# Optimization experiments

Hardware: AMD Instinct MI355X
Metric: run time of the kernel (lower is better)

## Reference

```python
import jax, jax.numpy as jnp
import numpy as np

SPATIAL_SHAPES = np.array([[128, 128], [64, 64], [32, 32], [16, 16]], dtype=np.int32)  # (H, W) per level
D_MODEL = 256
D_FFN = 1024
N_LEVELS = 4
N_HEADS = 8
N_POINTS = 4
HEAD_DIM = D_MODEL // N_HEADS
B = 2
LEN = int((SPATIAL_SHAPES[:, 0] * SPATIAL_SHAPES[:, 1]).sum())  # 21760


def layer_norm(x, g, b, eps=1e-5):
    mu = x.mean(-1, keepdims=True)
    var = ((x - mu) ** 2).mean(-1, keepdims=True)
    return (x - mu) / jnp.sqrt(var + eps) * g + b


def ms_deform_attn_core(value, sampling_locations, attention_weights):
    # value: [B, Len, M, D]; locations: [B, Lq, M, L, P, 2] in [0,1]; weights: [B, Lq, M, L, P]
    B_, _, M, D = value.shape
    Lq = sampling_locations.shape[1]
    P = sampling_locations.shape[4]
    out = jnp.zeros((B_, M, Lq, D), value.dtype)
    start = 0
    for lvl, (H, W) in enumerate(SPATIAL_SHAPES.tolist()):
        v = value[:, start:start + H * W].transpose(0, 2, 1, 3)  # [B, M, H*W, D]
        start += H * W
        loc = sampling_locations[:, :, :, lvl].transpose(0, 2, 1, 3, 4)  # [B, M, Lq, P, 2]
        # grid_sample semantics: align_corners=False, padding_mode='zeros'
        x = loc[..., 0] * W - 0.5
        y = loc[..., 1] * H - 0.5
        x0 = jnp.floor(x)
        y0 = jnp.floor(y)
        wx = (x - x0)[..., None]
        wy = (y - y0)[..., None]

        def gather(xi, yi):
            valid = ((xi >= 0) & (xi < W) & (yi >= 0) & (yi < H)).astype(value.dtype)
            idx = (jnp.clip(yi, 0, H - 1) * W + jnp.clip(xi, 0, W - 1)).astype(jnp.int32)
            idx = idx.reshape(B_, M, Lq * P)
            g = jnp.take_along_axis(v, idx[..., None], axis=2).reshape(B_, M, Lq, P, D)
            return g * valid[..., None]

        v00 = gather(x0, y0)
        v01 = gather(x0 + 1, y0)
        v10 = gather(x0, y0 + 1)
        v11 = gather(x0 + 1, y0 + 1)
        samp = (v00 * (1 - wx) + v01 * wx) * (1 - wy) + (v10 * (1 - wx) + v11 * wx) * wy
        w_l = attention_weights[:, :, :, lvl].transpose(0, 2, 1, 3)  # [B, M, Lq, P]
        out = out + (samp * w_l[..., None]).sum(axis=3)
    return out.transpose(0, 2, 1, 3).reshape(B_, Lq, M * D)


def setup_inputs() -> dict:
    key = jax.random.key(0)
    ks = jax.random.split(key, 16)
    f32 = jnp.float32

    def lin(k, fan_in, fan_out, scale=None):
        s = scale if scale is not None else 1.0 / np.sqrt(fan_in)
        return jax.random.normal(k, (fan_in, fan_out), f32) * s

    starts = np.concatenate([[0], np.cumsum(SPATIAL_SHAPES[:, 0] * SPATIAL_SHAPES[:, 1])[:-1]]).astype(np.int32)
    inp = {
        "src": jax.random.normal(ks[0], (B, LEN, D_MODEL), f32),
        "pos": jax.random.normal(ks[1], (B, LEN, D_MODEL), f32),
        "reference_points": jax.random.uniform(ks[2], (B, LEN, N_LEVELS, 2), f32),
        "spatial_shapes": jnp.asarray(SPATIAL_SHAPES),
        "level_start_index": jnp.asarray(starts),
        "norm1_g": jnp.ones((D_MODEL,), f32), "norm1_b": jnp.zeros((D_MODEL,), f32),
        "norm2_g": jnp.ones((D_MODEL,), f32), "norm2_b": jnp.zeros((D_MODEL,), f32),
        "W_value": lin(ks[3], D_MODEL, D_MODEL), "b_value": jnp.zeros((D_MODEL,), f32),
        "W_off": lin(ks[4], D_MODEL, N_HEADS * N_LEVELS * N_POINTS * 2, scale=0.01),
        "b_off": jax.random.normal(ks[5], (N_HEADS * N_LEVELS * N_POINTS * 2,), f32) * 0.01,
        "W_attn": lin(ks[6], D_MODEL, N_HEADS * N_LEVELS * N_POINTS),
        "b_attn": jnp.zeros((N_HEADS * N_LEVELS * N_POINTS,), f32),
        "W_out": lin(ks[7], D_MODEL, D_MODEL), "b_out": jnp.zeros((D_MODEL,), f32),
        "W_ffn1": lin(ks[8], D_MODEL, D_FFN), "b_ffn1": jnp.zeros((D_FFN,), f32),
        "W_ffn2": lin(ks[9], D_FFN, D_MODEL), "b_ffn2": jnp.zeros((D_MODEL,), f32),
    }
    return inp


def reference(src, pos, reference_points, spatial_shapes, level_start_index,
              norm1_g, norm1_b, norm2_g, norm2_b,
              W_value, b_value, W_off, b_off, W_attn, b_attn, W_out, b_out,
              W_ffn1, b_ffn1, W_ffn2, b_ffn2):
    B_, Lq, C = src.shape
    # pre-norm deformable self-attention; NOTE: value path uses un-normed src (faithful to source)
    q = layer_norm(src, norm1_g, norm1_b) + pos
    value = (src @ W_value + b_value).reshape(B_, Lq, N_HEADS, HEAD_DIM)
    offsets = (q @ W_off + b_off).reshape(B_, Lq, N_HEADS, N_LEVELS, N_POINTS, 2)
    attn = jax.nn.softmax((q @ W_attn + b_attn).reshape(B_, Lq, N_HEADS, N_LEVELS * N_POINTS), axis=-1)
    attn = attn.reshape(B_, Lq, N_HEADS, N_LEVELS, N_POINTS)
    offset_normalizer = spatial_shapes[..., ::-1].astype(src.dtype)  # (W, H) per level
    loc = reference_points[:, :, None, :, None, :] + offsets / offset_normalizer[None, None, None, :, None, :]
    attn_out = ms_deform_attn_core(value, loc, attn) @ W_out + b_out
    src = src + attn_out
    h = layer_norm(src, norm2_g, norm2_b)
    h = jax.nn.gelu(h @ W_ffn1 + b_ffn1, approximate=False) @ W_ffn2 + b_ffn2
    return src + h
```

## Files before the change

### kernel.cpp

```cpp
#include <hip/hip_runtime.h>
#include <hip/hip_bf16.h>
#include <math.h>

#define LEN_TOT 21760
#define BATCH 2
#define MROWS (BATCH * LEN_TOT)
#define DMODEL 256
#define DFFN 1024

typedef unsigned short ushort_t;
typedef __attribute__((ext_vector_type(8))) short short8;
typedef __attribute__((ext_vector_type(4))) float floatx4;
typedef __attribute__((address_space(3))) ushort_t lds_us;
typedef __attribute__((address_space(1))) const ushort_t glb_us;

__device__ __forceinline__ ushort_t f2b(float f) {
    unsigned u = __float_as_uint(f);
    unsigned r = (u + 0x7FFFu + ((u >> 16) & 1u)) >> 16;
    return (ushort_t)r;
}
__device__ __forceinline__ float b2f(ushort_t u) {
    return __uint_as_float(((unsigned)u) << 16);
}

struct TP {
    const float* s[6];
    ushort_t*    d[6];
    int K[6];
    int N[6];
    int start[7];
};

__global__ __launch_bounds__(256) void transpose_convert(TP tp) {
    __shared__ float tile[32][33];
    int blk = blockIdx.x;
    int seg = 0;
    while (seg < 5 && blk >= tp.start[seg + 1]) seg++;
    int local = blk - tp.start[seg];
    int K = tp.K[seg], N = tp.N[seg];
    int tn = N >> 5;
    int k0 = (local / tn) << 5, n0 = (local % tn) << 5;
    int r = threadIdx.x >> 5, c = threadIdx.x & 31;
    const float* src = tp.s[seg];
    #pragma unroll
    for (int rr = r; rr < 32; rr += 8)
        tile[rr][c] = src[(size_t)(k0 + rr) * N + n0 + c];
    __syncthreads();
    ushort_t* dst = tp.d[seg];
    #pragma unroll
    for (int rr = r; rr < 32; rr += 8)
        dst[(size_t)(n0 + rr) * K + k0 + c] = f2b(tile[c][rr]);
}

__global__ __launch_bounds__(256) void ln_dual_kernel(
    const float* __restrict__ x, const float* __restrict__ g,
    const float* __restrict__ bb, const float* __restrict__ addv,
    ushort_t* __restrict__ y_bf, ushort_t* __restrict__ x_bf)
{
    int row  = blockIdx.x * 4 + (threadIdx.x >> 6);
    int lane = threadIdx.x & 63;
    size_t base = (size_t)row * DMODEL + lane * 4;
    float4 v = *(const float4*)(x + base);

    float s = v.x + v.y + v.z + v.w;
    #pragma unroll
    for (int o = 32; o; o >>= 1) s += __shfl_xor(s, o, 64);
    float mu = s * (1.0f / 256.0f);

    float d0 = v.x - mu, d1 = v.y - mu, d2 = v.z - mu, d3 = v.w - mu;
    float vs = d0*d0 + d1*d1 + d2*d2 + d3*d3;
    #pragma unroll
    for (int o = 32; o; o >>= 1) vs += __shfl_xor(vs, o, 64);
    float rstd = rsqrtf(vs * (1.0f / 256.0f) + 1e-5f);

    float4 gv = *(const float4*)(g  + lane * 4);
    float4 bv = *(const float4*)(bb + lane * 4);
    float o0 = d0 * rstd * gv.x + bv.x;
    float o1 = d1 * rstd * gv.y + bv.y;
    float o2 = d2 * rstd * gv.z + bv.z;
    float o3 = d3 * rstd * gv.w + bv.w;
    if (addv) {
        float4 av = *(const float4*)(addv + base);
        o0 += av.x; o1 += av.y; o2 += av.z; o3 += av.w;
    }
    ushort4 ob = {f2b(o0), f2b(o1), f2b(o2), f2b(o3)};
    *(ushort4*)(y_bf + base) = ob;
    if (x_bf) {
        ushort4 xb = {f2b(v.x), f2b(v.y), f2b(v.z), f2b(v.w)};
        *(ushort4*)(x_bf + base) = xb;
    }
}

template<int GELU_ACT, int HAS_RES, int OUT_BF16>
__global__ __launch_bounds__(256) void gemm_mfma(
    const ushort_t* __restrict__ A, const ushort_t* __restrict__ Bt,
    const float* __restrict__ bias, const float* __restrict__ bias2, int bsplit,
    const float* __restrict__ res,
    float* __restrict__ C, ushort_t* __restrict__ Cbf,
    int M, int N, int K)
{
    constexpr int BM = 128, BK = 32;
    __shared__ __align__(16) ushort_t As[BM * BK];
    __shared__ __align__(16) ushort_t Bs[BM * BK];

    const int tid  = threadIdx.x;
    const int wave = tid >> 6;
    const int lane = tid & 63;
    const int wm = (wave & 1) * 64;
    const int wn = (wave >> 1) * 64;
    const int ml = lane & 15;
    const int quad = lane >> 4;
    const int m0 = blockIdx.y * BM, n0 = blockIdx.x * BM;

    const int r0 = tid >> 2, s0 = tid & 3;
    const int r1 = (tid + 256) >> 2;

    floatx4 acc[4][4] = {};

    for (int k0 = 0; k0 < K; k0 += BK) {
        const ushort_t* gA0 = A  + (size_t)(m0 + r0) * K + k0 + s0 * 8;
        const ushort_t* gA1 = A  + (size_t)(m0 + r1) * K + k0 + s0 * 8;
        const ushort_t* gB0 = Bt + (size_t)(n0 + r0) * K + k0 + s0 * 8;
        const ushort_t* gB1 = Bt + (size_t)(n0 + r1) * K + k0 + s0 * 8;
        __builtin_amdgcn_global_load_lds((glb_us*)gA0, (lds_us*)(As + tid * 8),        16, 0, 0);
        __builtin_amdgcn_global_load_lds((glb_us*)gA1, (lds_us*)(As + (tid + 256) * 8),16, 0, 0);
        __builtin_amdgcn_global_load_lds((glb_us*)gB0, (lds_us*)(Bs + tid * 8),        16, 0, 0);
        __builtin_amdgcn_global_load_lds((glb_us*)gB1, (lds_us*)(Bs + (tid + 256) * 8),16, 0, 0);
        __syncthreads();

        short8 af[4], bfr[4];
        #pragma unroll
        for (int i = 0; i < 4; i++)
            af[i] = *(const short8*)(As + (wm + i * 16 + ml) * BK + quad * 8);
        #pragma unroll
        for (int j = 0; j < 4; j++)
            bfr[j] = *(const short8*)(Bs + (wn + j * 16 + ml) * BK + quad * 8);
        #pragma unroll
        for (int i = 0; i < 4; i++)
            #pragma unroll
            for (int j = 0; j < 4; j++)
                acc[i][j] = __builtin_amdgcn_mfma_f32_16x16x32_bf16(
                    af[i], bfr[j], acc[i][j], 0, 0, 0);
        __syncthreads();
    }

    if (OUT_BF16) {
        ushort_t* pool  = (wave < 2) ? As : Bs;
        ushort_t* wbase = pool + (wave & 1) * 2048;
        const int lr  = lane >> 2;
        const int sg  = lane & 3;
        #pragma unroll
        for (int i = 0; i < 4; i++) {
            ushort_t* wbuf = wbase + (i & 1) * 1024;
            #pragma unroll
            for (int j = 0; j < 4; j++) {
                int col = n0 + wn + j * 16 + ml;
                float bc = (col < bsplit) ? bias[col] : bias2[col - bsplit];
                #pragma unroll
                for (int r = 0; r < 4; r++) {
                    float v = acc[i][j][r] + bc;
                    if (GELU_ACT) v = 0.5f * v * (1.0f + erff(v * 0.7071067811865476f));
                    if (HAS_RES)
                        v += res[(size_t)(m0 + wm + i * 16 + quad * 4 + r) * N
                                 + n0 + wn + j * 16 + ml];
                    wbuf[(quad * 4 + r) * 64 + j * 16 + ml] = f2b(v);
                }
            }
            asm volatile("s_waitcnt lgkmcnt(0)" ::: "memory");
            #pragma unroll
            for (int h = 0; h < 2; h++) {
                short8 vv = *(const short8*)(wbuf + lr * 64 + (sg + 4 * h) * 8);
                *(short8*)(Cbf + (size_t)(m0 + wm + i * 16 + lr) * N
                                 + n0 + wn + (sg + 4 * h) * 8) = vv;
            }
        }
    } else {
        #pragma unroll
        for (int j = 0; j < 4; j++) {
            int col = n0 + wn + j * 16 + ml;
            float bc = (col < bsplit) ? bias[col] : bias2[col - bsplit];
            #pragma unroll
            for (int i = 0; i < 4; i++) {
                int row = m0 + wm + i * 16 + quad * 4;
                #pragma unroll
                for (int r = 0; r < 4; r++) {
                    float v = acc[i][j][r] + bc;
                    if (GELU_ACT) v = 0.5f * v * (1.0f + erff(v * 0.7071067811865476f));
                    if (HAS_RES) v += res[(size_t)(row + r) * N + col];
                    C[(size_t)(row + r) * N + col] = v;
                }
            }
        }
    }
}

__global__ __launch_bounds__(256) void msdeform_kernel(
    const ushort_t* __restrict__ value, const float* __restrict__ comb,
    const float* __restrict__ refp, ushort_t* __restrict__ out_bf)
{
    int gid = blockIdx.x * 8 + (threadIdx.x >> 5);
    int l   = threadIdx.x & 31;
    int bq  = gid >> 3;
    int m   = gid & 7;
    int b   = (bq >= LEN_TOT) ? 1 : 0;

    int i = l & 15;
    float logit = comb[(size_t)bq * 384 + 256 + m * 16 + i];
    float mx = logit;
    #pragma unroll
    for (int o = 8; o; o >>= 1) mx = fmaxf(mx, __shfl_xor(mx, o, 32));
    float e = __expf(logit - mx);
    float se = e;
    #pragma unroll
    for (int o = 8; o; o >>= 1) se += __shfl_xor(se, o, 32);
    float prob = e / se;

    int lvl = i >> 2;
    int Wl  = 128 >> lvl;
    float Wf = (float)Wl;
    const int ST_[4] = {0, 16384, 20480, 21504};

    float2 off2 = ((const float2*)comb)[(size_t)bq * 192 + m * 16 + i];
    float2 ref2 = ((const float2*)refp)[(size_t)bq * 4 + lvl];
    float xs = fmaf(ref2.x, Wf, off2.x) - 0.5f;
    float ys = fmaf(ref2.y, Wf, off2.y) - 0.5f;
    float xf = floorf(xs), yf = floorf(ys);
    int x0 = (int)xf, y0 = (int)yf;
    float wx = xs - xf, wy = ys - yf;
    float wx1 = 1.0f - wx, wy1 = 1.0f - wy;

    bool vx0 = (x0 >= 0) & (x0 < Wl);
    bool vx1 = (x0 + 1 >= 0) & (x0 + 1 < Wl);
    bool vy0 = (y0 >= 0) & (y0 < Wl);
    bool vy1 = (y0 + 1 >= 0) & (y0 + 1 < Wl);
    int cx0 = min(max(x0, 0), Wl - 1);
    int cx1 = min(max(x0 + 1, 0), Wl - 1);
    int cy0 = min(max(y0, 0), Wl - 1);
    int cy1 = min(max(y0 + 1, 0), Wl - 1);

    int vbase = b * LEN_TOT + ST_[lvl];
    int i00 = (vbase + cy0 * Wl + cx0) * 256 + m * 32;
    int i01 = (vbase + cy0 * Wl + cx1) * 256 + m * 32;
    int i10 = (vbase + cy1 * Wl + cx0) * 256 + m * 32;
    int i11 = (vbase + cy1 * Wl + cx1) * 256 + m * 32;
    float w00 = (vx0 && vy0) ? prob * wx1 * wy1 : 0.0f;
    float w01 = (vx1 && vy0) ? prob * wx  * wy1 : 0.0f;
    float w10 = (vx0 && vy1) ? prob * wx1 * wy  : 0.0f;
    float w11 = (vx1 && vy1) ? prob * wx  * wy  : 0.0f;

    int sA = l >> 2;
    int cA = l & 3;
    int t0 = __shfl(i00, sA, 32), t1 = __shfl(i01, sA, 32);
    int t2 = __shfl(i10, sA, 32), t3 = __shfl(i11, sA, 32);
    int addrA = (cA == 0) ? t0 : (cA == 1) ? t1 : (cA == 2) ? t2 : t3;
    float u0 = __shfl(w00, sA, 32), u1 = __shfl(w01, sA, 32);
    float u2 = __shfl(w10, sA, 32), u3 = __shfl(w11, sA, 32);
    float wA = (cA == 0) ? u0 : (cA == 1) ? u1 : (cA == 2) ? u2 : u3;
    t0 = __shfl(i00, sA + 8, 32); t1 = __shfl(i01, sA + 8, 32);
    t2 = __shfl(i10, sA + 8, 32); t3 = __shfl(i11, sA + 8, 32);
    int addrB = (cA == 0) ? t0 : (cA == 1) ? t1 : (cA == 2) ? t2 : t3;
    u0 = __shfl(w00, sA + 8, 32); u1 = __shfl(w01, sA + 8, 32);
    u2 = __shfl(w10, sA + 8, 32); u3 = __shfl(w11, sA + 8, 32);
    float wB = (cA == 0) ? u0 : (cA == 1) ? u1 : (cA == 2) ? u2 : u3;

    int cl = l >> 3;
    int d4 = l & 7;
    float ax = 0.0f, ay = 0.0f, az = 0.0f, aw = 0.0f;
    #pragma unroll
    for (int s = 0; s < 8; s++) {
        int   a = __shfl(addrA, s * 4 + cl, 32);
        float w = __shfl(wA,    s * 4 + cl, 32);
        ushort4 v = *(const ushort4*)(value + a + (d4 << 2));
        ax = fmaf(w, b2f(v.x), ax); ay = fmaf(w, b2f(v.y), ay);
        az = fmaf(w, b2f(v.z), az); aw = fmaf(w, b2f(v.w), aw);
    }
    #pragma unroll
    for (int s = 0; s < 8; s++) {
        int   a = __shfl(addrB, s * 4 + cl, 32);
        float w = __shfl(wB,    s * 4 + cl, 32);
        ushort4 v = *(const ushort4*)(value + a + (d4 << 2));
        ax = fmaf(w, b2f(v.x), ax); ay = fmaf(w, b2f(v.y), ay);
        az = fmaf(w, b2f(v.z), az); aw = fmaf(w, b2f(v.w), aw);
    }
    ax += __shfl_xor(ax, 8, 32);  ay += __shfl_xor(ay, 8, 32);
    az += __shfl_xor(az, 8, 32);  aw += __shfl_xor(aw, 8, 32);
    ax += __shfl_xor(ax, 16, 32); ay += __shfl_xor(ay, 16, 32);
    az += __shfl_xor(az, 16, 32); aw += __shfl_xor(aw, 16, 32);

    if (l < 8) {
        ushort4 o = {f2b(ax), f2b(ay), f2b(az), f2b(aw)};
        *(ushort4*)(out_bf + (size_t)gid * 32 + (d4 << 2)) = o;
    }
}

extern "C" void kernel_launch(void* const* d_in, const int* in_sizes, int n_in,
                              void* d_out, int out_size, void* d_ws, size_t ws_size,
                              hipStream_t stream)
{
    const float* src  = (const float*)d_in[0];
    const float* pos  = (const float*)d_in[1];
    const float* refp = (const float*)d_in[2];
    const float* n1g = (const float*)d_in[5];
    const float* n1b = (const float*)d_in[6];
    const float* n2g = (const float*)d_in[7];
    const float* n2b = (const float*)d_in[8];
    const float* Wv  = (const float*)d_in[9];
    const float* bv  = (const float*)d_in[10];
    const float* Wof = (const float*)d_in[11];
    const float* bof = (const float*)d_in[12];
    const float* Wat = (const float*)d_in[13];
    const float* bat = (const float*)d_in[14];
    const float* Wo  = (const float*)d_in[15];
    const float* bo  = (const float*)d_in[16];
    const float* Wf1 = (const float*)d_in[17];
    const float* bf1 = (const float*)d_in[18];
    const float* Wf2 = (const float*)d_in[19];
    const float* bf2 = (const float*)d_in[20];
    float* out = (float*)d_out;

    char* ws = (char*)d_ws;
    const int M = MROWS;
    const size_t SZ_BF = (size_t)M * 256 * 2;
    const size_t SZ_F  = (size_t)M * 256 * 4;
    const int BIG = 1 << 30;

    ushort_t* q_bf    = (ushort_t*)(ws);
    ushort_t* value_b = (ushort_t*)(ws + SZ_BF);
    ushort_t* src_bf  = (ushort_t*)(ws + SZ_BF + SZ_F);
    float*    comb    = (float*)   (ws + 2 * SZ_BF + SZ_F);
    ushort_t* h0_bf   = q_bf;
    ushort_t* sampled = src_bf;
    float*    src2    = (float*)   (ws + SZ_BF);
    ushort_t* h1_bf   = src_bf;
    char* wtp = ws + 2 * SZ_BF + 2 * SZ_F + (size_t)M * 128 * 4;
    ushort_t* WvT  = (ushort_t*)(wtp);
    ushort_t* WofT = WvT  + 256 * 256;
    ushort_t* WatT = WofT + 256 * 256;
    ushort_t* WoT  = WatT + 256 * 128;
    ushort_t* Wf1T = WoT  + 256 * 256;
    ushort_t* Wf2T = Wf1T + 256 * 1024;

    TP tp;
    tp.s[0] = Wv;  tp.d[0] = WvT;  tp.K[0] = 256;  tp.N[0] = 256;
    tp.s[1] = Wof; tp.d[1] = WofT; tp.K[1] = 256;  tp.N[1] = 256;
    tp.s[2] = Wat; tp.d[2] = WatT; tp.K[2] = 256;  tp.N[2] = 128;
    tp.s[3] = Wo;  tp.d[3] = WoT;  tp.K[3] = 256;  tp.N[3] = 256;
    tp.s[4] = Wf1; tp.d[4] = Wf1T; tp.K[4] = 256;  tp.N[4] = 1024;
    tp.s[5] = Wf2; tp.d[5] = Wf2T; tp.K[5] = 1024; tp.N[5] = 256;
    tp.start[0] = 0;   tp.start[1] = 64;  tp.start[2] = 128;
    tp.start[3] = 160; tp.start[4] = 224; tp.start[5] = 480; tp.start[6] = 736;
    transpose_convert<<<736, 256, 0, stream>>>(tp);

    ln_dual_kernel<<<M / 4, 256, 0, stream>>>(src, n1g, n1b, pos, q_bf, src_bf);
    gemm_mfma<0, 0, 1><<<dim3(2, M / 128), 256, 0, stream>>>(
        src_bf, WvT, bv, bv, BIG, nullptr, nullptr, value_b, M, 256, 256);
    gemm_mfma<0, 0, 0><<<dim3(3, M / 128), 256, 0, stream>>>(
        q_bf, WofT, bof, bat, 256, nullptr, comb, nullptr, M, 384, 256);
    msdeform_kernel<<<M, 256, 0, stream>>>(value_b, comb, refp, sampled);
    gemm_mfma<0, 1, 0><<<dim3(2, M / 128), 256, 0, stream>>>(
        sampled, WoT, bo, bo, BIG, src, src2, nullptr, M, 256, 256);
    ln_dual_kernel<<<M / 4, 256, 0, stream>>>(src2, n2g, n2b, nullptr, h0_bf, nullptr);
    gemm_mfma<1, 0, 1><<<dim3(8, M / 128), 256, 0, stream>>>(
        h0_bf, Wf1T, bf1, bf1, BIG, nullptr, nullptr, h1_bf, M, 1024, 256);
    gemm_mfma<0, 1, 0><<<dim3(2, M / 128), 256, 0, stream>>>(
        h1_bf, Wf2T, bf2, bf2, BIG, src2, out, nullptr, M, 256, 1024);
}
```

Before: 500.3 us.

## Store value head-major and fetch horizontal bilinear pairs with single 16-byte loads

```diff
diff --git a/kernel.cpp b/kernel.cpp
--- a/kernel.cpp
+++ b/kernel.cpp
@@ -91,7 +91,7 @@
     }
 }
 
-template<int GELU_ACT, int HAS_RES, int OUT_BF16>
+template<int GELU_ACT, int HAS_RES, int OUT_BF16, int HEADMAJ>
 __global__ __launch_bounds__(256) void gemm_mfma(
     const ushort_t* __restrict__ A, const ushort_t* __restrict__ Bt,
     const float* __restrict__ bias, const float* __restrict__ bias2, int bsplit,
@@ -170,8 +170,13 @@
             #pragma unroll
             for (int h = 0; h < 2; h++) {
                 short8 vv = *(const short8*)(wbuf + lr * 64 + (sg + 4 * h) * 8);
-                *(short8*)(Cbf + (size_t)(m0 + wm + i * 16 + lr) * N
-                                 + n0 + wn + (sg + 4 * h) * 8) = vv;
+                size_t row = (size_t)(m0 + wm + i * 16 + lr);
+                int    col = n0 + wn + (sg + 4 * h) * 8;
+                if (HEADMAJ) {
+                    *(short8*)(Cbf + ((size_t)(col >> 5) * M + row) * 32 + (col & 31)) = vv;
+                } else {
+                    *(short8*)(Cbf + row * N + col) = vv;
+                }
             }
         }
     } else {
@@ -205,6 +210,8 @@
     int b   = (bq >= LEN_TOT) ? 1 : 0;
 
     int i = l & 15;
+    int r = l >> 4;
+
     float logit = comb[(size_t)bq * 384 + 256 + m * 16 + i];
     float mx = logit;
     #pragma unroll
@@ -227,69 +234,59 @@
     float xf = floorf(xs), yf = floorf(ys);
     int x0 = (int)xf, y0 = (int)yf;
     float wx = xs - xf, wy = ys - yf;
-    float wx1 = 1.0f - wx, wy1 = 1.0f - wy;
-
-    bool vx0 = (x0 >= 0) & (x0 < Wl);
-    bool vx1 = (x0 + 1 >= 0) & (x0 + 1 < Wl);
-    bool vy0 = (y0 >= 0) & (y0 < Wl);
-    bool vy1 = (y0 + 1 >= 0) & (y0 + 1 < Wl);
-    int cx0 = min(max(x0, 0), Wl - 1);
-    int cx1 = min(max(x0 + 1, 0), Wl - 1);
-    int cy0 = min(max(y0, 0), Wl - 1);
-    int cy1 = min(max(y0 + 1, 0), Wl - 1);
-
-    int vbase = b * LEN_TOT + ST_[lvl];
-    int i00 = (vbase + cy0 * Wl + cx0) * 256 + m * 32;
-    int i01 = (vbase + cy0 * Wl + cx1) * 256 + m * 32;
-    int i10 = (vbase + cy1 * Wl + cx0) * 256 + m * 32;
-    int i11 = (vbase + cy1 * Wl + cx1) * 256 + m * 32;
-    float w00 = (vx0 && vy0) ? prob * wx1 * wy1 : 0.0f;
-    float w01 = (vx1 && vy0) ? prob * wx  * wy1 : 0.0f;
-    float w10 = (vx0 && vy1) ? prob * wx1 * wy  : 0.0f;
-    float w11 = (vx1 && vy1) ? prob * wx  * wy  : 0.0f;
-
-    int sA = l >> 2;
-    int cA = l & 3;
-    int t0 = __shfl(i00, sA, 32), t1 = __shfl(i01, sA, 32);
-    int t2 = __shfl(i10, sA, 32), t3 = __shfl(i11, sA, 32);
-    int addrA = (cA == 0) ? t0 : (cA == 1) ? t1 : (cA == 2) ? t2 : t3;
-    float u0 = __shfl(w00, sA, 32), u1 = __shfl(w01, sA, 32);
-    float u2 = __shfl(w10, sA, 32), u3 = __shfl(w11, sA, 32);
-    float wA = (cA == 0) ? u0 : (cA == 1) ? u1 : (cA == 2) ? u2 : u3;
-    t0 = __shfl(i00, sA + 8, 32); t1 = __shfl(i01, sA + 8, 32);
-    t2 = __shfl(i10, sA + 8, 32); t3 = __shfl(i11, sA + 8, 32);
-    int addrB = (cA == 0) ? t0 : (cA == 1) ? t1 : (cA == 2) ? t2 : t3;
-    u0 = __shfl(w00, sA + 8, 32); u1 = __shfl(w01, sA + 8, 32);
-    u2 = __shfl(w10, sA + 8, 32); u3 = __shfl(w11, sA + 8, 32);
-    float wB = (cA == 0) ? u0 : (cA == 1) ? u1 : (cA == 2) ? u2 : u3;
-
-    int cl = l >> 3;
-    int d4 = l & 7;
-    float ax = 0.0f, ay = 0.0f, az = 0.0f, aw = 0.0f;
-    #pragma unroll
-    for (int s = 0; s < 8; s++) {
-        int   a = __shfl(addrA, s * 4 + cl, 32);
-        float w = __shfl(wA,    s * 4 + cl, 32);
-        ushort4 v = *(const ushort4*)(value + a + (d4 << 2));
-        ax = fmaf(w, b2f(v.x), ax); ay = fmaf(w, b2f(v.y), ay);
-        az = fmaf(w, b2f(v.z), az); aw = fmaf(w, b2f(v.w), aw);
-    }
-    #pragma unroll
-    for (int s = 0; s < 8; s++) {
-        int   a = __shfl(addrB, s * 4 + cl, 32);
-        float w = __shfl(wB,    s * 4 + cl, 32);
-        ushort4 v = *(const ushort4*)(value + a + (d4 << 2));
-        ax = fmaf(w, b2f(v.x), ax); ay = fmaf(w, b2f(v.y), ay);
-        az = fmaf(w, b2f(v.z), az); aw = fmaf(w, b2f(v.w), aw);
-    }
-    ax += __shfl_xor(ax, 8, 32);  ay += __shfl_xor(ay, 8, 32);
-    az += __shfl_xor(az, 8, 32);  aw += __shfl_xor(aw, 8, 32);
-    ax += __shfl_xor(ax, 16, 32); ay += __shfl_xor(ay, 16, 32);
-    az += __shfl_xor(az, 16, 32); aw += __shfl_xor(aw, 16, 32);
-
-    if (l < 8) {
-        ushort4 o = {f2b(ax), f2b(ay), f2b(az), f2b(aw)};
-        *(ushort4*)(out_bf + (size_t)gid * 32 + (d4 << 2)) = o;
+
+    int xb = min(max(x0, 0), Wl - 2);
+    int s0 = (x0 == xb) ? 0 : 1;
+    float c0w = ((x0 >= 0) & (x0 < Wl))         ? (1.0f - wx) : 0.0f;
+    float c1w = ((x0 + 1 >= 0) & (x0 + 1 < Wl)) ? wx          : 0.0f;
+
+    int yc = y0 + r;
+    bool vy = (yc >= 0) & (yc < Wl);
+    int cyc = min(max(yc, 0), Wl - 1);
+    float wyr = r ? wy : (1.0f - wy);
+    float pw = vy ? prob * wyr : 0.0f;
+
+    float wc0 = pw * c0w, wc1 = pw * c1w;
+    float hwA = s0 ? wc1 : wc0;
+    float hwB = s0 ? wc0 : wc1;
+
+    int addrP = (m * MROWS + b * LEN_TOT + ST_[lvl] + cyc * Wl + xb) * 32;
+
+    const int pr = l >> 3;
+    const int bl = l & 7;
+    float a0=0,a1=0,a2=0,a3=0,a4=0,a5=0,a6=0,a7=0;
+    #pragma unroll
+    for (int it = 0; it < 8; it++) {
+        int p = it * 4 + pr;
+        int   a  = __shfl(addrP, p, 32);
+        float hA = __shfl(hwA, p, 32);
+        float hB = __shfl(hwB, p, 32);
+        float h  = (bl & 4) ? hB : hA;
+        uint4 u = *(const uint4*)(value + a + bl * 8);
+        a0 = fmaf(h, __uint_as_float(u.x << 16),          a0);
+        a1 = fmaf(h, __uint_as_float(u.x & 0xffff0000u),  a1);
+        a2 = fmaf(h, __uint_as_float(u.y << 16),          a2);
+        a3 = fmaf(h, __uint_as_float(u.y & 0xffff0000u),  a3);
+        a4 = fmaf(h, __uint_as_float(u.z << 16),          a4);
+        a5 = fmaf(h, __uint_as_float(u.z & 0xffff0000u),  a5);
+        a6 = fmaf(h, __uint_as_float(u.w << 16),          a6);
+        a7 = fmaf(h, __uint_as_float(u.w & 0xffff0000u),  a7);
+    }
+    #pragma unroll
+    for (int o = 4; o <= 16; o <<= 1) {
+        a0 += __shfl_xor(a0, o, 32); a1 += __shfl_xor(a1, o, 32);
+        a2 += __shfl_xor(a2, o, 32); a3 += __shfl_xor(a3, o, 32);
+        a4 += __shfl_xor(a4, o, 32); a5 += __shfl_xor(a5, o, 32);
+        a6 += __shfl_xor(a6, o, 32); a7 += __shfl_xor(a7, o, 32);
+    }
+
+    if (l < 4) {
+        short8 ov;
+        ov[0] = (short)f2b(a0); ov[1] = (short)f2b(a1);
+        ov[2] = (short)f2b(a2); ov[3] = (short)f2b(a3);
+        ov[4] = (short)f2b(a4); ov[5] = (short)f2b(a5);
+        ov[6] = (short)f2b(a6); ov[7] = (short)f2b(a7);
+        *(short8*)(out_bf + (size_t)gid * 32 + l * 8) = ov;
     }
 }
 
@@ -352,16 +349,16 @@
     transpose_convert<<<736, 256, 0, stream>>>(tp);
 
     ln_dual_kernel<<<M / 4, 256, 0, stream>>>(src, n1g, n1b, pos, q_bf, src_bf);
-    gemm_mfma<0, 0, 1><<<dim3(2, M / 128), 256, 0, stream>>>(
+    gemm_mfma<0, 0, 1, 1><<<dim3(2, M / 128), 256, 0, stream>>>(
         src_bf, WvT, bv, bv, BIG, nullptr, nullptr, value_b, M, 256, 256);
-    gemm_mfma<0, 0, 0><<<dim3(3, M / 128), 256, 0, stream>>>(
+    gemm_mfma<0, 0, 0, 0><<<dim3(3, M / 128), 256, 0, stream>>>(
         q_bf, WofT, bof, bat, 256, nullptr, comb, nullptr, M, 384, 256);
     msdeform_kernel<<<M, 256, 0, stream>>>(value_b, comb, refp, sampled);
-    gemm_mfma<0, 1, 0><<<dim3(2, M / 128), 256, 0, stream>>>(
+    gemm_mfma<0, 1, 0, 0><<<dim3(2, M / 128), 256, 0, stream>>>(
         sampled, WoT, bo, bo, BIG, src, src2, nullptr, M, 256, 256);
     ln_dual_kernel<<<M / 4, 256, 0, stream>>>(src2, n2g, n2b, nullptr, h0_bf, nullptr);
-    gemm_mfma<1, 0, 1><<<dim3(8, M / 128), 256, 0, stream>>>(
+    gemm_mfma<1, 0, 1, 0><<<dim3(8, M / 128), 256, 0, stream>>>(
         h0_bf, Wf1T, bf1, bf1, BIG, nullptr, nullptr, h1_bf, M, 1024, 256);
-    gemm_mfma<0, 1, 0><<<dim3(2, M / 128), 256, 0, stream>>>(
+    gemm_mfma<0, 1, 0, 0><<<dim3(2, M / 128), 256, 0, stream>>>(
         h1_bf, Wf2T, bf2, bf2, BIG, src2, out, nullptr, M, 256, 1024);
 }
```

Result: slower. 512.1 us (+2.4%).
